# Performance work log

Measured on AMD Instinct MI355X. Metric: run time of the kernel, lower is better.

Reference implementation:

```python
import jax, jax.numpy as jnp
import numpy as np

B, S, D, H = 2, 2048, 2048, 16
HD = D // H  # head_dim = 128
ROPE_THETA = 10000.0
NEG = -1e9


def _rotate_half(x):
    x1, x2 = jnp.split(x, 2, axis=-1)
    return jnp.concatenate([-x2, x1], axis=-1)


def setup_inputs() -> dict:
    key = jax.random.key(0)
    ks = jax.random.split(key, 6)
    scale = 1.0 / np.sqrt(D)
    hidden_states = jax.random.normal(ks[0], (B, S, D), dtype=jnp.float32)
    # additive causal mask: 0 on/below diagonal, large negative above
    causal = jnp.triu(jnp.full((S, S), NEG, dtype=jnp.float32), k=1)
    attention_mask = jnp.broadcast_to(causal[None, None], (B, 1, S, S))
    position_ids = jnp.broadcast_to(jnp.arange(S, dtype=jnp.int64)[None], (B, S))
    Wq = jax.random.normal(ks[1], (D, D), dtype=jnp.float32) * scale
    Wk = jax.random.normal(ks[2], (D, D), dtype=jnp.float32) * scale
    Wv = jax.random.normal(ks[3], (D, D), dtype=jnp.float32) * scale
    Wo = jax.random.normal(ks[4], (D, D), dtype=jnp.float32) * scale
    return dict(hidden_states=hidden_states, attention_mask=attention_mask,
                position_ids=position_ids, Wq=Wq, Wk=Wk, Wv=Wv, Wo=Wo)


def reference(hidden_states, attention_mask, position_ids, Wq, Wk, Wv, Wo):
    b, s, d = hidden_states.shape
    # projections (weights stored [in, out])
    q = (hidden_states @ Wq).reshape(b, s, H, HD).transpose(0, 2, 1, 3)  # bhsd
    k = (hidden_states @ Wk).reshape(b, s, H, HD).transpose(0, 2, 1, 3)
    v = (hidden_states @ Wv).reshape(b, s, H, HD).transpose(0, 2, 1, 3)
    # rotary embeddings
    inv_freq = 1.0 / (ROPE_THETA ** (jnp.arange(0, HD, 2, dtype=jnp.float32) / HD))
    freqs = position_ids.astype(jnp.float32)[..., None] * inv_freq  # [b, s, HD/2]
    emb = jnp.concatenate([freqs, freqs], axis=-1)
    cos = jnp.cos(emb)[:, None]  # [b, 1, s, HD]
    sin = jnp.sin(emb)[:, None]
    q = q * cos + _rotate_half(q) * sin
    k = k * cos + _rotate_half(k) * sin
    # attention
    scores = jnp.einsum('bhqd,bhkd->bhqk', q, k) / jnp.sqrt(jnp.float32(HD))
    scores = scores + attention_mask
    probs = jax.nn.softmax(scores.astype(jnp.float32), axis=-1).astype(q.dtype)
    out = jnp.einsum('bhqk,bhkd->bhqd', probs, v)
    out = out.transpose(0, 2, 1, 3).reshape(b, s, d)
    return out @ Wo
```

## Files before the change

### kernel.cpp

```cpp
#include <hip/hip_runtime.h>
#include <hip/hip_bf16.h>

#define Bv 2
#define Sv 2048
#define Dv 2048
#define Hv 16
#define HDv 128

typedef short bf16x8 __attribute__((ext_vector_type(8)));
typedef float f32x4 __attribute__((ext_vector_type(4)));

__device__ inline float b2f(unsigned short u) {
  union { unsigned int i; float f; } x; x.i = ((unsigned int)u) << 16; return x.f;
}
__device__ inline unsigned short f2b(float f) {
  union { float f; unsigned int u; } x; x.f = f;
  unsigned int r = (x.u + 0x7fffu + ((x.u >> 16) & 1u)) >> 16;
  return (unsigned short)r;
}

#define GLL16(gsrc, ldst)                                                      \
  __builtin_amdgcn_global_load_lds(                                            \
      (__attribute__((address_space(1))) void*)(gsrc),                         \
      (__attribute__((address_space(3))) void*)(ldst), 16, 0, 0)

__global__ __launch_bounds__(256) void f2b_kernel(const float4* __restrict__ in,
                                                  ushort4* __restrict__ out, int n4) {
  int i = blockIdx.x * 256 + threadIdx.x;
  if (i >= n4) return;
  float4 v = in[i];
  ushort4 r;
  r.x = f2b(v.x); r.y = f2b(v.y); r.z = f2b(v.z); r.w = f2b(v.w);
  out[i] = r;
}

__global__ void wtrans_kernel(const float* __restrict__ W, short* __restrict__ WT) {
  __shared__ float tile[32][33];
  int tx = threadIdx.x, ty = threadIdx.y;
  int c0 = blockIdx.x * 32, r0 = blockIdx.y * 32;
#pragma unroll
  for (int i = 0; i < 4; i++)
    tile[ty + i * 8][tx] = W[(long)(r0 + ty + i * 8) * Dv + c0 + tx];
  __syncthreads();
#pragma unroll
  for (int i = 0; i < 4; i++)
    WT[(long)(c0 + ty + i * 8) * Dv + r0 + tx] = (short)f2b(tile[tx][ty + i * 8]);
}

__global__ void vtrans_kernel(const short* __restrict__ V, short* __restrict__ VT) {
  __shared__ short tile[32][33];
  int tx = threadIdx.x, ty = threadIdx.y;
  int k0 = blockIdx.x * 32, d0 = blockIdx.y * 32, bh = blockIdx.z;
  const short* src = V + (long)bh * Sv * HDv;
  short* dst = VT + (long)bh * HDv * Sv;
#pragma unroll
  for (int i = 0; i < 4; i++)
    tile[ty + i * 8][tx] = src[(long)(k0 + ty + i * 8) * HDv + d0 + tx];
  __syncthreads();
#pragma unroll
  for (int i = 0; i < 4; i++)
    dst[(long)(d0 + ty + i * 8) * Sv + k0 + tx] = tile[tx][ty + i * 8];
}

__global__ __launch_bounds__(256) void rope_table_kernel(float* __restrict__ tab) {
  int i = blockIdx.x * 256 + threadIdx.x;
  int s = i >> 6, d = i & 63;
  float inv = powf(10000.f, -(float)d * (1.f / 64.f));
  float ang = (float)s * inv;
  tab[s * 128 + d] = cosf(ang);
  tab[s * 128 + 64 + d] = sinf(ang);
}

__global__ __launch_bounds__(256) void rope_kernel(short* __restrict__ T,
                                                   const float* __restrict__ tab) {
  int tid = blockIdx.x * 256 + threadIdx.x;
  int r = tid >> 3, j = tid & 7;
  int s = r & (Sv - 1);
  short* p = T + (long)r * HDv + j * 8;
  bf16x8 a = *(const bf16x8*)p;
  bf16x8 bb = *(const bf16x8*)(p + 64);
  const float* tc = tab + s * 128 + j * 8;
  float4 c0 = *(const float4*)tc, c1 = *(const float4*)(tc + 4);
  float4 s0 = *(const float4*)(tc + 64), s1 = *(const float4*)(tc + 68);
  float cs[8] = {c0.x, c0.y, c0.z, c0.w, c1.x, c1.y, c1.z, c1.w};
  float sn[8] = {s0.x, s0.y, s0.z, s0.w, s1.x, s1.y, s1.z, s1.w};
  bf16x8 na, nb;
#pragma unroll
  for (int e = 0; e < 8; e++) {
    float x1 = b2f((unsigned short)a[e]);
    float x2 = b2f((unsigned short)bb[e]);
    na[e] = (short)f2b(x1 * cs[e] - x2 * sn[e]);
    nb[e] = (short)f2b(x2 * cs[e] + x1 * sn[e]);
  }
  *(bf16x8*)p = na;
  *(bf16x8*)(p + 64) = nb;
}

template <int MODE>
__global__ __launch_bounds__(256) void gemm_kernel(const short* __restrict__ A,
                                                   const short* __restrict__ Bt,
                                                   void* __restrict__ Cout,
                                                   int M, int N, int K) {
  __shared__ __align__(16) short As[128 * 32];
  __shared__ __align__(16) short Bs[128 * 32];
  const int t = threadIdx.x, w = t >> 6, l = t & 63;
  const int m0 = blockIdx.y * 128, n0 = blockIdx.x * 128;
  const int wr = w >> 1, wc = w & 1;
  f32x4 acc[4][4] = {};
  const short* ag = A + (long)(m0 + (t >> 2)) * K + (t & 3) * 8;
  const short* bg = Bt + (long)(n0 + (t >> 2)) * K + (t & 3) * 8;
  short* asw = As + (w * 16) * 32;
  short* bsw = Bs + (w * 16) * 32;
  const int aoff = (wr * 64 + (l & 15)) * 32 + (l >> 4) * 8;
  const int boff = (wc * 64 + (l & 15)) * 32 + (l >> 4) * 8;
  for (int k0 = 0; k0 < K; k0 += 32) {
    GLL16(ag + k0, asw);
    GLL16(ag + (long)64 * K + k0, asw + 64 * 32);
    GLL16(bg + k0, bsw);
    GLL16(bg + (long)64 * K + k0, bsw + 64 * 32);
    __syncthreads();
    bf16x8 af[4], bf[4];
#pragma unroll
    for (int i = 0; i < 4; i++) af[i] = *(const bf16x8*)(As + aoff + i * 16 * 32);
#pragma unroll
    for (int i = 0; i < 4; i++) bf[i] = *(const bf16x8*)(Bs + boff + i * 16 * 32);
#pragma unroll
    for (int i = 0; i < 4; i++)
#pragma unroll
      for (int j = 0; j < 4; j++)
        acc[i][j] = __builtin_amdgcn_mfma_f32_16x16x32_bf16(af[i], bf[j], acc[i][j], 0, 0, 0);
    __syncthreads();
  }
  const int fr = l >> 4;
#pragma unroll
  for (int mi = 0; mi < 4; mi++) {
#pragma unroll
    for (int ni = 0; ni < 4; ni++) {
      f32x4 v = acc[mi][ni];
      int col = n0 + wc * 64 + ni * 16 + (l & 15);
      int mbase = m0 + wr * 64 + mi * 16 + fr * 4;
      if (MODE == 0) {
        short* qkv = (short*)Cout;
        int which = col >> 11, hn = col & 2047;
        int h = hn >> 7, d = hn & 127;
#pragma unroll
        for (int j = 0; j < 4; j++) {
          int m = mbase + j;
          int b = m >> 11, s = m & 2047;
          qkv[(long)which * 8388608 + (((long)(b * Hv + h)) * Sv + s) * HDv + d] =
              (short)f2b(v[j]);
        }
      } else {
        float* C = (float*)Cout;
#pragma unroll
        for (int j = 0; j < 4; j++) C[(long)(mbase + j) * N + col] = v[j];
      }
    }
  }
}

__global__ __launch_bounds__(256, 2) void attn_kernel(const short* __restrict__ Q,
                                                      const short* __restrict__ Kk,
                                                      const short* __restrict__ VT,
                                                      short* __restrict__ O) {
  __shared__ __align__(16) short k_s[2][64 * 128];
  __shared__ __align__(16) short vt_s[2][64 * 128];
  __shared__ __align__(16) short p_s[4][2][16 * 64];
  const int t = threadIdx.x, w = t >> 6, l = t & 63;
  const int g = l >> 4, a = l & 15;
  const int bh = blockIdx.y;
  const int qb = ((bh >> 4) & 1) ? blockIdx.x : (15 - blockIdx.x);
  const int q0 = qb * 128;
  const short* Qb = Q + (long)bh * Sv * HDv;
  const short* Kb = Kk + (long)bh * Sv * HDv;
  const short* VTb = VT + (long)bh * HDv * Sv;
  const int rr = l >> 4, sub = l & 15;

  bf16x8 qf[2][4];
#pragma unroll
  for (int m = 0; m < 2; m++)
#pragma unroll
    for (int kk = 0; kk < 4; kk++)
      qf[m][kk] = *(const bf16x8*)(Qb + (long)(q0 + m * 64 + w * 16 + a) * HDv + kk * 32 + g * 8);

  f32x4 acc_o[2][8] = {};
  float m_run[2][4] = {{-1e30f, -1e30f, -1e30f, -1e30f}, {-1e30f, -1e30f, -1e30f, -1e30f}};
  float l_run[2][4] = {};
  const float scale = 0.08838834764831845f;
  const int kbmax = 2 * qb + 1;

#define STAGE_TILE(kdst, vdst, kv0_)                                              \
  {                                                                               \
    _Pragma("unroll") for (int j = 0; j < 4; j++) {                               \
      int row = j * 16 + w * 4 + rr;                                              \
      int c0 = (sub * 8) ^ ((row & 15) << 3);                                     \
      GLL16(Kb + (long)((kv0_) + row) * HDv + c0, (kdst) + (j * 16 + w * 4) * 128); \
    }                                                                             \
    _Pragma("unroll") for (int j = 0; j < 4; j++) {                               \
      int row = w * 16 + j * 4 + rr;                                              \
      int c0 = (sub * 8) ^ ((row & 15) << 3);                                     \
      int d = row + (c0 & 64);                                                    \
      GLL16(VTb + (long)d * Sv + (kv0_) + (c0 & 63), (vdst) + (w * 16 + j * 4) * 128); \
    }                                                                             \
  }

  STAGE_TILE(k_s[0], vt_s[0], 0);

  for (int kb = 0; kb <= kbmax; ++kb) {
    const int cur = kb & 1;
    const int kv0 = kb * 64;
    if (kb < kbmax) {
      STAGE_TILE(k_s[cur ^ 1], vt_s[cur ^ 1], kv0 + 64);
      asm volatile("s_waitcnt vmcnt(8)" ::: "memory");
    } else {
      asm volatile("s_waitcnt vmcnt(0)" ::: "memory");
    }
    __builtin_amdgcn_s_barrier();
    __builtin_amdgcn_sched_barrier(0);
    const short* ks = k_s[cur];
    const short* vs = vt_s[cur];
#pragma unroll
    for (int m = 0; m < 2; m++) {
      if (m == 0 && kb == kbmax) continue;
      f32x4 sacc[4] = {};
#pragma unroll
      for (int ksb = 0; ksb < 4; ksb++) {
        int row = ksb * 16 + a;
#pragma unroll
        for (int kk = 0; kk < 4; kk++) {
          bf16x8 kf = *(const bf16x8*)(ks + row * 128 + ((kk * 32 + g * 8) ^ ((row & 15) << 3)));
          sacc[ksb] = __builtin_amdgcn_mfma_f32_16x16x32_bf16(qf[m][kk], kf, sacc[ksb], 0, 0, 0);
        }
      }
      const bool domask = (kb == 2 * qb + m);
      float s[4][4];
#pragma unroll
      for (int ksb = 0; ksb < 4; ksb++)
#pragma unroll
        for (int r = 0; r < 4; r++) {
          float v = sacc[ksb][r] * scale;
          if (domask) {
            int key = kv0 + ksb * 16 + a, qq = q0 + m * 64 + w * 16 + g * 4 + r;
            v = (key <= qq) ? v : -1e30f;
          }
          s[ksb][r] = v;
        }
      float mnew[4], alpha[4];
#pragma unroll
      for (int r = 0; r < 4; r++) {
        float mm = fmaxf(fmaxf(s[0][r], s[1][r]), fmaxf(s[2][r], s[3][r]));
        mm = fmaxf(mm, __shfl_xor(mm, 1));
        mm = fmaxf(mm, __shfl_xor(mm, 2));
        mm = fmaxf(mm, __shfl_xor(mm, 4));
        mm = fmaxf(mm, __shfl_xor(mm, 8));
        mnew[r] = fmaxf(m_run[m][r], mm);
        alpha[r] = __expf(m_run[m][r] - mnew[r]);
        m_run[m][r] = mnew[r];
      }
      float rs[4] = {0.f, 0.f, 0.f, 0.f};
#pragma unroll
      for (int ksb = 0; ksb < 4; ksb++)
#pragma unroll
        for (int r = 0; r < 4; r++) {
          float p = __expf(s[ksb][r] - mnew[r]);
          s[ksb][r] = p;
          rs[r] += p;
        }
#pragma unroll
      for (int r = 0; r < 4; r++) {
        float x = rs[r];
        x += __shfl_xor(x, 1);
        x += __shfl_xor(x, 2);
        x += __shfl_xor(x, 4);
        x += __shfl_xor(x, 8);
        l_run[m][r] = l_run[m][r] * alpha[r] + x;
      }
#pragma unroll
      for (int ksb = 0; ksb < 4; ksb++)
#pragma unroll
        for (int r = 0; r < 4; r++) {
          int q_loc = g * 4 + r;
          p_s[w][m][q_loc * 64 + ((ksb * 16 + a) ^ ((q_loc & 7) << 3))] =
              (short)f2b(s[ksb][r]);
        }
#pragma unroll
      for (int d = 0; d < 8; d++)
#pragma unroll
        for (int r = 0; r < 4; r++) acc_o[m][d][r] *= alpha[r];
      bf16x8 pa[2];
#pragma unroll
      for (int kc = 0; kc < 2; kc++)
        pa[kc] = *(const bf16x8*)(&p_s[w][m][a * 64 + ((kc * 32 + g * 8) ^ ((a & 7) << 3))]);
#pragma unroll
      for (int dblk = 0; dblk < 8; dblk++) {
        int row = (dblk & 3) * 16 + a;
        int half = (dblk >> 2) * 64;
#pragma unroll
        for (int kc = 0; kc < 2; kc++) {
          bf16x8 vf = *(const bf16x8*)(vs + row * 128 +
                                       ((half + kc * 32 + g * 8) ^ ((row & 15) << 3)));
          acc_o[m][dblk] = __builtin_amdgcn_mfma_f32_16x16x32_bf16(pa[kc], vf, acc_o[m][dblk], 0, 0, 0);
        }
      }
    }
    __builtin_amdgcn_sched_barrier(0);
    __builtin_amdgcn_s_barrier();
  }
  const int b = bh >> 4, h = bh & 15;
#pragma unroll
  for (int m = 0; m < 2; m++)
#pragma unroll
    for (int r = 0; r < 4; r++) {
      float inv = 1.f / l_run[m][r];
      int q = q0 + m * 64 + w * 16 + g * 4 + r;
      short* orow = O + ((long)(b * Sv + q)) * Dv + h * HDv + a;
#pragma unroll
      for (int d = 0; d < 8; d++) orow[d * 16] = (short)f2b(acc_o[m][d][r] * inv);
    }
#undef STAGE_TILE
}

extern "C" void kernel_launch(void* const* d_in, const int* in_sizes, int n_in,
                              void* d_out, int out_size, void* d_ws, size_t ws_size,
                              hipStream_t stream) {
  const float* X = (const float*)d_in[0];
  const float* Wq = (const float*)d_in[3];
  const float* Wk = (const float*)d_in[4];
  const float* Wv = (const float*)d_in[5];
  const float* Wo = (const float*)d_in[6];
  float* out = (float*)d_out;

  short* XB = (short*)d_ws;
  short* WQKVT = XB + 8388608;
  short* WOT = WQKVT + 12582912;
  short* QKV = WOT + 4194304;
  float* TAB = (float*)(QKV + 25165824);
  short* AO = XB;
  short* VTG = WQKVT;

  f2b_kernel<<<8192, 256, 0, stream>>>((const float4*)X, (ushort4*)XB, 2097152);
  dim3 wtb(32, 8), wtg(64, 64);
  wtrans_kernel<<<wtg, wtb, 0, stream>>>(Wq, WQKVT);
  wtrans_kernel<<<wtg, wtb, 0, stream>>>(Wk, WQKVT + 4194304);
  wtrans_kernel<<<wtg, wtb, 0, stream>>>(Wv, WQKVT + 8388608);
  wtrans_kernel<<<wtg, wtb, 0, stream>>>(Wo, WOT);
  rope_table_kernel<<<512, 256, 0, stream>>>(TAB);
  gemm_kernel<0><<<dim3(48, 32), 256, 0, stream>>>(XB, WQKVT, QKV, 4096, 6144, 2048);
  rope_kernel<<<4096, 256, 0, stream>>>(QKV, TAB);
  vtrans_kernel<<<dim3(64, 4, 32), wtb, 0, stream>>>(QKV + 16777216, VTG);
  attn_kernel<<<dim3(16, 32), 256, 0, stream>>>(QKV, QKV + 8388608, VTG, AO);
  gemm_kernel<1><<<dim3(16, 32), 256, 0, stream>>>(AO, WOT, out, 4096, 2048, 2048);
}
```

Baseline: 512.5 us.

## Write V transposed from QKV GEMM and pair causal query tiles per block

The QKV projection epilogue now writes V directly in [bh, d, s] layout, which removes the separate V transpose kernel and its extra global round trip. The attention kernel is also restructured: each block now handles two 64-row query tiles, one from the far end and one from the near end (31-x and x), run one after the other. This gives every block the same 33 KV iterations under the causal mask instead of the earlier uneven 128-row tile scheme, and halves the register state per warp. The cost is strided, uncoalesced 2-byte stores for V in the GEMM epilogue, plus a serial dependency between the two query tiles within a block.

Measured after the change: 481.4 us. -6.1%, faster.

```diff
diff --git a/kernel.cpp b/kernel.cpp
--- a/kernel.cpp
+++ b/kernel.cpp
@@ -45,21 +45,6 @@
 #pragma unroll
   for (int i = 0; i < 4; i++)
     WT[(long)(c0 + ty + i * 8) * Dv + r0 + tx] = (short)f2b(tile[tx][ty + i * 8]);
-}
-
-__global__ void vtrans_kernel(const short* __restrict__ V, short* __restrict__ VT) {
-  __shared__ short tile[32][33];
-  int tx = threadIdx.x, ty = threadIdx.y;
-  int k0 = blockIdx.x * 32, d0 = blockIdx.y * 32, bh = blockIdx.z;
-  const short* src = V + (long)bh * Sv * HDv;
-  short* dst = VT + (long)bh * HDv * Sv;
-#pragma unroll
-  for (int i = 0; i < 4; i++)
-    tile[ty + i * 8][tx] = src[(long)(k0 + ty + i * 8) * HDv + d0 + tx];
-  __syncthreads();
-#pragma unroll
-  for (int i = 0; i < 4; i++)
-    dst[(long)(d0 + ty + i * 8) * Sv + k0 + tx] = tile[tx][ty + i * 8];
 }
 
 __global__ __launch_bounds__(256) void rope_table_kernel(float* __restrict__ tab) {
@@ -147,8 +132,13 @@
         for (int j = 0; j < 4; j++) {
           int m = mbase + j;
           int b = m >> 11, s = m & 2047;
-          qkv[(long)which * 8388608 + (((long)(b * Hv + h)) * Sv + s) * HDv + d] =
-              (short)f2b(v[j]);
+          if (which == 2) {
+            qkv[(long)2 * 8388608 + ((long)(b * Hv + h) * HDv + d) * Sv + s] =
+                (short)f2b(v[j]);
+          } else {
+            qkv[(long)which * 8388608 + (((long)(b * Hv + h)) * Sv + s) * HDv + d] =
+                (short)f2b(v[j]);
+          }
         }
       } else {
         float* C = (float*)Cout;
@@ -165,29 +155,31 @@
                                                       short* __restrict__ O) {
   __shared__ __align__(16) short k_s[2][64 * 128];
   __shared__ __align__(16) short vt_s[2][64 * 128];
-  __shared__ __align__(16) short p_s[4][2][16 * 64];
-  const int t = threadIdx.x, w = t >> 6, l = t & 63;
+  __shared__ __align__(16) short p_s[4][16 * 64];
+  const int tid = threadIdx.x, w = tid >> 6, l = tid & 63;
   const int g = l >> 4, a = l & 15;
   const int bh = blockIdx.y;
-  const int qb = ((bh >> 4) & 1) ? blockIdx.x : (15 - blockIdx.x);
-  const int q0 = qb * 128;
+  const int x = blockIdx.x;
+  const int qbH = 31 - x, qbL = x;
+  const int nb = 32 - x;
   const short* Qb = Q + (long)bh * Sv * HDv;
   const short* Kb = Kk + (long)bh * Sv * HDv;
   const short* VTb = VT + (long)bh * HDv * Sv;
   const int rr = l >> 4, sub = l & 15;
 
-  bf16x8 qf[2][4];
-#pragma unroll
-  for (int m = 0; m < 2; m++)
-#pragma unroll
-    for (int kk = 0; kk < 4; kk++)
-      qf[m][kk] = *(const bf16x8*)(Qb + (long)(q0 + m * 64 + w * 16 + a) * HDv + kk * 32 + g * 8);
-
-  f32x4 acc_o[2][8] = {};
-  float m_run[2][4] = {{-1e30f, -1e30f, -1e30f, -1e30f}, {-1e30f, -1e30f, -1e30f, -1e30f}};
-  float l_run[2][4] = {};
+  bf16x8 qfA[4], qfB[4];
+#pragma unroll
+  for (int kk = 0; kk < 4; kk++) {
+    qfA[kk] = *(const bf16x8*)(Qb + (long)(qbH * 64 + w * 16 + a) * HDv + kk * 32 + g * 8);
+    qfB[kk] = *(const bf16x8*)(Qb + (long)(qbL * 64 + w * 16 + a) * HDv + kk * 32 + g * 8);
+  }
+
+  f32x4 acc_o[8] = {};
+  float m_run[4] = {-1e30f, -1e30f, -1e30f, -1e30f};
+  float l_run[4] = {0.f, 0.f, 0.f, 0.f};
+  int qcur = qbH;
   const float scale = 0.08838834764831845f;
-  const int kbmax = 2 * qb + 1;
+  const int b = bh >> 4, h = bh & 15;
 
 #define STAGE_TILE(kdst, vdst, kv0_)                                              \
   {                                                                               \
@@ -204,120 +196,128 @@
     }                                                                             \
   }
 
+#define WRITE_OUT(qbv)                                                            \
+  {                                                                               \
+    _Pragma("unroll") for (int r = 0; r < 4; r++) {                               \
+      float inv = 1.f / l_run[r];                                                 \
+      int q = (qbv) * 64 + w * 16 + g * 4 + r;                                    \
+      short* orow = O + ((long)(b * Sv + q)) * Dv + h * HDv + a;                  \
+      _Pragma("unroll") for (int d = 0; d < 8; d++)                               \
+        orow[d * 16] = (short)f2b(acc_o[d][r] * inv);                             \
+    }                                                                             \
+  }
+
   STAGE_TILE(k_s[0], vt_s[0], 0);
 
-  for (int kb = 0; kb <= kbmax; ++kb) {
-    const int cur = kb & 1;
-    const int kv0 = kb * 64;
-    if (kb < kbmax) {
-      STAGE_TILE(k_s[cur ^ 1], vt_s[cur ^ 1], kv0 + 64);
+  for (int t = 0; t <= 32; ++t) {
+    const int cur = t & 1;
+    const int kv0 = (t < nb) ? t * 64 : (t - nb) * 64;
+    if (t < 32) {
+      const int nk = ((t + 1) < nb) ? (t + 1) * 64 : (t + 1 - nb) * 64;
+      STAGE_TILE(k_s[cur ^ 1], vt_s[cur ^ 1], nk);
       asm volatile("s_waitcnt vmcnt(8)" ::: "memory");
     } else {
       asm volatile("s_waitcnt vmcnt(0)" ::: "memory");
     }
     __builtin_amdgcn_s_barrier();
     __builtin_amdgcn_sched_barrier(0);
+    if (t == nb) {
+      WRITE_OUT(qbH);
+#pragma unroll
+      for (int kk = 0; kk < 4; kk++) qfA[kk] = qfB[kk];
+#pragma unroll
+      for (int d = 0; d < 8; d++) acc_o[d] = (f32x4){0.f, 0.f, 0.f, 0.f};
+#pragma unroll
+      for (int r = 0; r < 4; r++) { m_run[r] = -1e30f; l_run[r] = 0.f; }
+      qcur = qbL;
+    }
     const short* ks = k_s[cur];
     const short* vs = vt_s[cur];
-#pragma unroll
-    for (int m = 0; m < 2; m++) {
-      if (m == 0 && kb == kbmax) continue;
-      f32x4 sacc[4] = {};
-#pragma unroll
-      for (int ksb = 0; ksb < 4; ksb++) {
-        int row = ksb * 16 + a;
-#pragma unroll
-        for (int kk = 0; kk < 4; kk++) {
-          bf16x8 kf = *(const bf16x8*)(ks + row * 128 + ((kk * 32 + g * 8) ^ ((row & 15) << 3)));
-          sacc[ksb] = __builtin_amdgcn_mfma_f32_16x16x32_bf16(qf[m][kk], kf, sacc[ksb], 0, 0, 0);
+    f32x4 sacc[4] = {};
+#pragma unroll
+    for (int ksb = 0; ksb < 4; ksb++) {
+      int row = ksb * 16 + a;
+#pragma unroll
+      for (int kk = 0; kk < 4; kk++) {
+        bf16x8 kf = *(const bf16x8*)(ks + row * 128 + ((kk * 32 + g * 8) ^ ((row & 15) << 3)));
+        sacc[ksb] = __builtin_amdgcn_mfma_f32_16x16x32_bf16(qfA[kk], kf, sacc[ksb], 0, 0, 0);
+      }
+    }
+    const bool domask = (t == nb - 1) || (t == 32);
+    float s[4][4];
+#pragma unroll
+    for (int ksb = 0; ksb < 4; ksb++)
+#pragma unroll
+      for (int r = 0; r < 4; r++) {
+        float v = sacc[ksb][r] * scale;
+        if (domask) {
+          int key = kv0 + ksb * 16 + a, qq = qcur * 64 + w * 16 + g * 4 + r;
+          v = (key <= qq) ? v : -1e30f;
         }
-      }
-      const bool domask = (kb == 2 * qb + m);
-      float s[4][4];
-#pragma unroll
-      for (int ksb = 0; ksb < 4; ksb++)
-#pragma unroll
-        for (int r = 0; r < 4; r++) {
-          float v = sacc[ksb][r] * scale;
-          if (domask) {
-            int key = kv0 + ksb * 16 + a, qq = q0 + m * 64 + w * 16 + g * 4 + r;
-            v = (key <= qq) ? v : -1e30f;
-          }
-          s[ksb][r] = v;
-        }
-      float mnew[4], alpha[4];
+        s[ksb][r] = v;
+      }
+    float mnew[4], alpha[4];
+#pragma unroll
+    for (int r = 0; r < 4; r++) {
+      float mm = fmaxf(fmaxf(s[0][r], s[1][r]), fmaxf(s[2][r], s[3][r]));
+      mm = fmaxf(mm, __shfl_xor(mm, 1));
+      mm = fmaxf(mm, __shfl_xor(mm, 2));
+      mm = fmaxf(mm, __shfl_xor(mm, 4));
+      mm = fmaxf(mm, __shfl_xor(mm, 8));
+      mnew[r] = fmaxf(m_run[r], mm);
+      alpha[r] = __expf(m_run[r] - mnew[r]);
+      m_run[r] = mnew[r];
+    }
+    float rs[4] = {0.f, 0.f, 0.f, 0.f};
+#pragma unroll
+    for (int ksb = 0; ksb < 4; ksb++)
 #pragma unroll
       for (int r = 0; r < 4; r++) {
-        float mm = fmaxf(fmaxf(s[0][r], s[1][r]), fmaxf(s[2][r], s[3][r]));
-        mm = fmaxf(mm, __shfl_xor(mm, 1));
-        mm = fmaxf(mm, __shfl_xor(mm, 2));
-        mm = fmaxf(mm, __shfl_xor(mm, 4));
-        mm = fmaxf(mm, __shfl_xor(mm, 8));
-        mnew[r] = fmaxf(m_run[m][r], mm);
-        alpha[r] = __expf(m_run[m][r] - mnew[r]);
-        m_run[m][r] = mnew[r];
-      }
-      float rs[4] = {0.f, 0.f, 0.f, 0.f};
-#pragma unroll
-      for (int ksb = 0; ksb < 4; ksb++)
-#pragma unroll
-        for (int r = 0; r < 4; r++) {
-          float p = __expf(s[ksb][r] - mnew[r]);
-          s[ksb][r] = p;
-          rs[r] += p;
-        }
+        float p = __expf(s[ksb][r] - mnew[r]);
+        s[ksb][r] = p;
+        rs[r] += p;
+      }
+#pragma unroll
+    for (int r = 0; r < 4; r++) {
+      float xx = rs[r];
+      xx += __shfl_xor(xx, 1);
+      xx += __shfl_xor(xx, 2);
+      xx += __shfl_xor(xx, 4);
+      xx += __shfl_xor(xx, 8);
+      l_run[r] = l_run[r] * alpha[r] + xx;
+    }
+#pragma unroll
+    for (int ksb = 0; ksb < 4; ksb++)
 #pragma unroll
       for (int r = 0; r < 4; r++) {
-        float x = rs[r];
-        x += __shfl_xor(x, 1);
-        x += __shfl_xor(x, 2);
-        x += __shfl_xor(x, 4);
-        x += __shfl_xor(x, 8);
-        l_run[m][r] = l_run[m][r] * alpha[r] + x;
-      }
-#pragma unroll
-      for (int ksb = 0; ksb < 4; ksb++)
-#pragma unroll
-        for (int r = 0; r < 4; r++) {
-          int q_loc = g * 4 + r;
-          p_s[w][m][q_loc * 64 + ((ksb * 16 + a) ^ ((q_loc & 7) << 3))] =
-              (short)f2b(s[ksb][r]);
-        }
-#pragma unroll
-      for (int d = 0; d < 8; d++)
-#pragma unroll
-        for (int r = 0; r < 4; r++) acc_o[m][d][r] *= alpha[r];
-      bf16x8 pa[2];
-#pragma unroll
-      for (int kc = 0; kc < 2; kc++)
-        pa[kc] = *(const bf16x8*)(&p_s[w][m][a * 64 + ((kc * 32 + g * 8) ^ ((a & 7) << 3))]);
-#pragma unroll
-      for (int dblk = 0; dblk < 8; dblk++) {
-        int row = (dblk & 3) * 16 + a;
-        int half = (dblk >> 2) * 64;
-#pragma unroll
-        for (int kc = 0; kc < 2; kc++) {
-          bf16x8 vf = *(const bf16x8*)(vs + row * 128 +
-                                       ((half + kc * 32 + g * 8) ^ ((row & 15) << 3)));
-          acc_o[m][dblk] = __builtin_amdgcn_mfma_f32_16x16x32_bf16(pa[kc], vf, acc_o[m][dblk], 0, 0, 0);
-        }
+        int q_loc = g * 4 + r;
+        p_s[w][q_loc * 64 + ((ksb * 16 + a) ^ ((q_loc & 7) << 3))] = (short)f2b(s[ksb][r]);
+      }
+#pragma unroll
+    for (int d = 0; d < 8; d++)
+#pragma unroll
+      for (int r = 0; r < 4; r++) acc_o[d][r] *= alpha[r];
+    bf16x8 pa[2];
+#pragma unroll
+    for (int kc = 0; kc < 2; kc++)
+      pa[kc] = *(const bf16x8*)(&p_s[w][a * 64 + ((kc * 32 + g * 8) ^ ((a & 7) << 3))]);
+#pragma unroll
+    for (int dblk = 0; dblk < 8; dblk++) {
+      int row = (dblk & 3) * 16 + a;
+      int half = (dblk >> 2) * 64;
+#pragma unroll
+      for (int kc = 0; kc < 2; kc++) {
+        bf16x8 vf = *(const bf16x8*)(vs + row * 128 +
+                                     ((half + kc * 32 + g * 8) ^ ((row & 15) << 3)));
+        acc_o[dblk] = __builtin_amdgcn_mfma_f32_16x16x32_bf16(pa[kc], vf, acc_o[dblk], 0, 0, 0);
       }
     }
     __builtin_amdgcn_sched_barrier(0);
     __builtin_amdgcn_s_barrier();
   }
-  const int b = bh >> 4, h = bh & 15;
-#pragma unroll
-  for (int m = 0; m < 2; m++)
-#pragma unroll
-    for (int r = 0; r < 4; r++) {
-      float inv = 1.f / l_run[m][r];
-      int q = q0 + m * 64 + w * 16 + g * 4 + r;
-      short* orow = O + ((long)(b * Sv + q)) * Dv + h * HDv + a;
-#pragma unroll
-      for (int d = 0; d < 8; d++) orow[d * 16] = (short)f2b(acc_o[m][d][r] * inv);
-    }
+  WRITE_OUT(qbL);
 #undef STAGE_TILE
+#undef WRITE_OUT
 }
 
 extern "C" void kernel_launch(void* const* d_in, const int* in_sizes, int n_in,
@@ -336,7 +336,6 @@
   short* QKV = WOT + 4194304;
   float* TAB = (float*)(QKV + 25165824);
   short* AO = XB;
-  short* VTG = WQKVT;
 
   f2b_kernel<<<8192, 256, 0, stream>>>((const float4*)X, (ushort4*)XB, 2097152);
   dim3 wtb(32, 8), wtg(64, 64);
@@ -347,7 +346,6 @@
   rope_table_kernel<<<512, 256, 0, stream>>>(TAB);
   gemm_kernel<0><<<dim3(48, 32), 256, 0, stream>>>(XB, WQKVT, QKV, 4096, 6144, 2048);
   rope_kernel<<<4096, 256, 0, stream>>>(QKV, TAB);
-  vtrans_kernel<<<dim3(64, 4, 32), wtb, 0, stream>>>(QKV + 16777216, VTG);
-  attn_kernel<<<dim3(16, 32), 256, 0, stream>>>(QKV, QKV + 8388608, VTG, AO);
+  attn_kernel<<<dim3(16, 32), 256, 0, stream>>>(QKV, QKV + 8388608, QKV + 16777216, AO);
   gemm_kernel<1><<<dim3(16, 32), 256, 0, stream>>>(AO, WOT, out, 4096, 2048, 2048);
 }
```
